# Kernel optimization log

Hardware: AMD Instinct MI355X
Metric: run time of the kernel (lower is better)

The kernel has to match this reference:

```python
import jax, jax.numpy as jnp
import numpy as np

N1, N2, C, H = 512, 512, 256, 512

def setup_inputs() -> dict:
    key = jax.random.key(0)
    ks = jax.random.split(key, 8)
    std = 0.01
    return {
        "X": jax.random.normal(ks[0], (N1, C), dtype=jnp.float32),
        "Y": jax.random.normal(ks[1], (N2, C), dtype=jnp.float32),
        "W_sr": jax.random.normal(ks[2], (C, C), dtype=jnp.float32) * std,   # project_sr.weight
        "W_tg": jax.random.normal(ks[3], (C, C), dtype=jnp.float32) * std,   # project_tg.weight
        "W1": jax.random.normal(ks[4], (H, 2 * C), dtype=jnp.float32) * std, # fc_M[0].weight [512,512]
        "b1": jnp.zeros((H,), dtype=jnp.float32),                            # fc_M[0].bias
        "w2": jax.random.normal(ks[5], (1, H), dtype=jnp.float32) * std,     # fc_M[2].weight [1,512]
        "b2": jnp.zeros((1,), dtype=jnp.float32),                            # fc_M[2].bias
    }

def reference(X, Y, W_sr, W_tg, W1, b1, w2, b2):
    # Projections (Linear without bias): x @ W.T
    Xp = X @ W_sr.T  # [N1, C]
    Yp = Y @ W_tg.T  # [N2, C]
    # fc_M first layer acts on concat([X_k, Y_k], -1); split W1 into the
    # halves that multiply Xp and Yp respectively (mathematically identical
    # to materializing the [N1,N2,2C] concat, but avoids it).
    W1x, W1y = W1[:, :C], W1[:, C:]
    hx = Xp @ W1x.T                     # [N1, H]
    hy = Yp @ W1y.T                     # [N2, H]
    Hid = jax.nn.relu(hx[:, None, :] + hy[None, :, :] + b1)  # [N1, N2, H]
    M = Hid @ w2[0] + b2[0]             # [N1, N2]  (squeeze of last dim 1)
    return M
```

## Files before the change

kernel.cpp:

```cpp
#include <hip/hip_runtime.h>


__global__ __launch_bounds__(256) void gemm_nt(
    const float* __restrict__ A0, const float* __restrict__ A1,
    const float* __restrict__ B0, const float* __restrict__ B1,
    float* __restrict__ C0, float* __restrict__ C1,
    const float* __restrict__ bias1, int N, int ldb)
{
    const int z = blockIdx.z;
    const float* A = z ? A1 : A0;
    const float* B = z ? B1 : B0;
    float* Cc      = z ? C1 : C0;
    const float* bias = z ? bias1 : nullptr;

    __shared__ float As[32 * 34];
    __shared__ float Bs[32 * 68];

    const int t  = threadIdx.x;
    const int m0 = blockIdx.x * 32;
    const int n0 = blockIdx.y * 64;
    const int ti = t / 16;
    const int tj = t % 16;

    float acc[2][4] = {};

    for (int kt = 0; kt < 256; kt += 32) {
        {
            const int m  = t / 8;
            const int k4 = (t % 8) * 4;
            float4 v = *(const float4*)&A[(m0 + m) * 256 + kt + k4];
            As[(k4 + 0) * 34 + m] = v.x;
            As[(k4 + 1) * 34 + m] = v.y;
            As[(k4 + 2) * 34 + m] = v.z;
            As[(k4 + 3) * 34 + m] = v.w;
        }
        #pragma unroll
        for (int r = 0; r < 2; r++) {
            const int id = t + r * 256;
            const int n  = id / 8;
            const int k4 = (id % 8) * 4;
            float4 v = *(const float4*)&B[(n0 + n) * ldb + kt + k4];
            Bs[(k4 + 0) * 68 + n] = v.x;
            Bs[(k4 + 1) * 68 + n] = v.y;
            Bs[(k4 + 2) * 68 + n] = v.z;
            Bs[(k4 + 3) * 68 + n] = v.w;
        }
        __syncthreads();

        #pragma unroll 8
        for (int k = 0; k < 32; k++) {
            float2 a = *(float2*)&As[k * 34 + 2 * ti];
            float4 b = *(float4*)&Bs[k * 68 + 4 * tj];
            acc[0][0] += a.x * b.x;  acc[0][1] += a.x * b.y;
            acc[0][2] += a.x * b.z;  acc[0][3] += a.x * b.w;
            acc[1][0] += a.y * b.x;  acc[1][1] += a.y * b.y;
            acc[1][2] += a.y * b.z;  acc[1][3] += a.y * b.w;
        }
        __syncthreads();
    }

    float4 bv = {0.f, 0.f, 0.f, 0.f};
    if (bias) bv = *(const float4*)&bias[n0 + 4 * tj];
    #pragma unroll
    for (int mi = 0; mi < 2; mi++) {
        const int m = m0 + 2 * ti + mi;
        float4 r;
        r.x = acc[mi][0] + bv.x;
        r.y = acc[mi][1] + bv.y;
        r.z = acc[mi][2] + bv.z;
        r.w = acc[mi][3] + bv.w;
        *(float4*)&Cc[m * N + n0 + 4 * tj] = r;
    }
}

__global__ __launch_bounds__(256) void affinity_core(
    const float* __restrict__ hx, const float* __restrict__ hy,
    const float* __restrict__ w2, float* __restrict__ partial)
{
    __shared__ float xs[64 * 68];
    __shared__ float ys[64 * 68];
    __shared__ float ws2[64];

    const int t  = threadIdx.x;
    const int i0 = blockIdx.x * 64;
    const int j0 = blockIdx.y * 64;
    const int h0 = blockIdx.z * 64;
    const int ti = t / 16;
    const int tj = t % 16;

    #pragma unroll
    for (int s = 0; s < 4; s++) {
        const int id = t + s * 256;
        const int r  = id / 16;
        const int c4 = (id % 16) * 4;
        *(float4*)&xs[r * 68 + c4] = *(const float4*)&hx[(i0 + r) * 512 + h0 + c4];
        *(float4*)&ys[r * 68 + c4] = *(const float4*)&hy[(j0 + r) * 512 + h0 + c4];
    }
    if (t < 16) *(float4*)&ws2[t * 4] = *(const float4*)&w2[h0 + t * 4];
    __syncthreads();

    float acc[4][4] = {};
    const float* xr = xs + ti * 68;
    const float* yr = ys + tj * 68;

    #pragma unroll 2
    for (int h4 = 0; h4 < 16; h4++) {
        const int ho = h4 * 4;
        float4 w = *(const float4*)&ws2[ho];
        float4 x[4], y[4];
        #pragma unroll
        for (int m = 0; m < 4; m++) x[m] = *(const float4*)&xr[m * (16 * 68) + ho];
        #pragma unroll
        for (int n = 0; n < 4; n++) y[n] = *(const float4*)&yr[n * (16 * 68) + ho];
        #pragma unroll
        for (int m = 0; m < 4; m++) {
            #pragma unroll
            for (int n = 0; n < 4; n++) {
                acc[m][n] += fmaxf(x[m].x + y[n].x, 0.f) * w.x
                           + fmaxf(x[m].y + y[n].y, 0.f) * w.y
                           + fmaxf(x[m].z + y[n].z, 0.f) * w.z
                           + fmaxf(x[m].w + y[n].w, 0.f) * w.w;
            }
        }
    }

    float* p = partial + blockIdx.z * (512 * 512);
    #pragma unroll
    for (int m = 0; m < 4; m++) {
        #pragma unroll
        for (int n = 0; n < 4; n++) {
            p[(i0 + ti + 16 * m) * 512 + (j0 + tj + 16 * n)] = acc[m][n];
        }
    }
}

__global__ __launch_bounds__(256) void reduce8(
    const float* __restrict__ partial, const float* __restrict__ b2,
    float* __restrict__ out)
{
    const int idx = (blockIdx.x * 256 + threadIdx.x) * 4;
    const float bb = b2[0];
    float4 r = {bb, bb, bb, bb};
    #pragma unroll
    for (int s = 0; s < 8; s++) {
        float4 p = *(const float4*)&partial[s * 262144 + idx];
        r.x += p.x; r.y += p.y; r.z += p.z; r.w += p.w;
    }
    *(float4*)&out[idx] = r;
}

extern "C" void kernel_launch(void* const* d_in, const int* in_sizes, int n_in,
                              void* d_out, int out_size, void* d_ws, size_t ws_size,
                              hipStream_t stream) {
    const float* X    = (const float*)d_in[0];
    const float* Y    = (const float*)d_in[1];
    const float* W_sr = (const float*)d_in[2];
    const float* W_tg = (const float*)d_in[3];
    const float* W1   = (const float*)d_in[4];
    const float* b1   = (const float*)d_in[5];
    const float* w2   = (const float*)d_in[6];
    const float* b2   = (const float*)d_in[7];

    float* ws      = (float*)d_ws;
    float* Xp      = ws;
    float* Yp      = ws + 131072;
    float* hx      = ws + 262144;
    float* hy      = ws + 524288;
    float* partial = ws + 786432;
    float* out     = (float*)d_out;

    gemm_nt<<<dim3(16, 4, 2), 256, 0, stream>>>(X, Y, W_sr, W_tg, Xp, Yp,
                                                nullptr, 256, 256);
    gemm_nt<<<dim3(16, 8, 2), 256, 0, stream>>>(Xp, Yp, W1, W1 + 256, hx, hy,
                                                b1, 512, 512);
    affinity_core<<<dim3(8, 8, 8), 256, 0, stream>>>(hx, hy, w2, partial);
    reduce8<<<256, 256, 0, stream>>>(partial, b2, out);
}
```

Before: 116.3 us.

## Fuse all four stages into one cooperative kernel with grid syncs

Replaces the four separate launches (two projection GEMMs, the affinity core and the partial reduction) with a single cooperative kernel of 256 blocks that runs each stage in turn, separated by grid-wide syncs. The affinity stage now gives each block 128 hidden units in two 64-wide chunks, so only four partial slabs are written and reduced instead of eight. The aim is to remove launch overhead and inter-kernel gaps and to cut partial-buffer traffic. In exchange, the affinity stage drops from 512 to 256 blocks with more serial work per block, and each grid sync adds a barrier cost.

Measured after the change: 212.4 us. 1.83x slower.

```diff
diff --git a/kernel.cpp b/kernel.cpp
--- a/kernel.cpp
+++ b/kernel.cpp
@@ -1,24 +1,19 @@
 #include <hip/hip_runtime.h>
-
-
-__global__ __launch_bounds__(256) void gemm_nt(
-    const float* __restrict__ A0, const float* __restrict__ A1,
-    const float* __restrict__ B0, const float* __restrict__ B1,
-    float* __restrict__ C0, float* __restrict__ C1,
-    const float* __restrict__ bias1, int N, int ldb)
+#include <hip/hip_cooperative_groups.h>
+
+namespace cg = cooperative_groups;
+
+
+#define LDS_FLOATS (2 * 64 * 68 + 64)
+
+__device__ __forceinline__ void gemm_tile_32x64(
+    const float* __restrict__ A, const float* __restrict__ B,
+    float* __restrict__ C, const float* __restrict__ bias,
+    int m0, int n0, int N, int ldb, float* lds, int t)
 {
-    const int z = blockIdx.z;
-    const float* A = z ? A1 : A0;
-    const float* B = z ? B1 : B0;
-    float* Cc      = z ? C1 : C0;
-    const float* bias = z ? bias1 : nullptr;
-
-    __shared__ float As[32 * 34];
-    __shared__ float Bs[32 * 68];
-
-    const int t  = threadIdx.x;
-    const int m0 = blockIdx.x * 32;
-    const int n0 = blockIdx.y * 64;
+    float* As = lds;
+    float* Bs = lds + 32 * 34;
+
     const int ti = t / 16;
     const int tj = t % 16;
 
@@ -69,84 +64,127 @@
         r.y = acc[mi][1] + bv.y;
         r.z = acc[mi][2] + bv.z;
         r.w = acc[mi][3] + bv.w;
-        *(float4*)&Cc[m * N + n0 + 4 * tj] = r;
+        *(float4*)&C[m * N + n0 + 4 * tj] = r;
     }
 }
 
-__global__ __launch_bounds__(256) void affinity_core(
-    const float* __restrict__ hx, const float* __restrict__ hy,
-    const float* __restrict__ w2, float* __restrict__ partial)
+__global__ __launch_bounds__(256) void fused_affinity(
+    const float* __restrict__ X, const float* __restrict__ Y,
+    const float* __restrict__ W_sr, const float* __restrict__ W_tg,
+    const float* __restrict__ W1, const float* __restrict__ b1,
+    const float* __restrict__ w2, const float* __restrict__ b2,
+    float* __restrict__ ws, float* __restrict__ out)
 {
-    __shared__ float xs[64 * 68];
-    __shared__ float ys[64 * 68];
-    __shared__ float ws2[64];
-
-    const int t  = threadIdx.x;
-    const int i0 = blockIdx.x * 64;
-    const int j0 = blockIdx.y * 64;
-    const int h0 = blockIdx.z * 64;
-    const int ti = t / 16;
-    const int tj = t % 16;
-
-    #pragma unroll
-    for (int s = 0; s < 4; s++) {
-        const int id = t + s * 256;
-        const int r  = id / 16;
-        const int c4 = (id % 16) * 4;
-        *(float4*)&xs[r * 68 + c4] = *(const float4*)&hx[(i0 + r) * 512 + h0 + c4];
-        *(float4*)&ys[r * 68 + c4] = *(const float4*)&hy[(j0 + r) * 512 + h0 + c4];
-    }
-    if (t < 16) *(float4*)&ws2[t * 4] = *(const float4*)&w2[h0 + t * 4];
-    __syncthreads();
-
-    float acc[4][4] = {};
-    const float* xr = xs + ti * 68;
-    const float* yr = ys + tj * 68;
-
-    #pragma unroll 2
-    for (int h4 = 0; h4 < 16; h4++) {
-        const int ho = h4 * 4;
-        float4 w = *(const float4*)&ws2[ho];
-        float4 x[4], y[4];
-        #pragma unroll
-        for (int m = 0; m < 4; m++) x[m] = *(const float4*)&xr[m * (16 * 68) + ho];
-        #pragma unroll
-        for (int n = 0; n < 4; n++) y[n] = *(const float4*)&yr[n * (16 * 68) + ho];
+    cg::grid_group grid = cg::this_grid();
+
+    __shared__ float lds[LDS_FLOATS];
+
+    float* Xp      = ws;
+    float* Yp      = ws + 131072;
+    float* hx      = ws + 262144;
+    float* hy      = ws + 524288;
+    float* partial = ws + 786432;
+
+    const int b = blockIdx.x;
+    const int t = threadIdx.x;
+
+    if (b < 128) {
+        const int prob = b >> 6;
+        const int tile = b & 63;
+        const int m0 = (tile >> 2) * 32;
+        const int n0 = (tile & 3) * 64;
+        gemm_tile_32x64(prob ? Y : X, prob ? W_tg : W_sr,
+                        prob ? Yp : Xp, nullptr,
+                        m0, n0, 256, 256, lds, t);
+    }
+    grid.sync();
+
+    {
+        const int prob = b >> 7;
+        const int tile = b & 127;
+        const int m0 = (tile >> 3) * 32;
+        const int n0 = (tile & 7) * 64;
+        gemm_tile_32x64(prob ? Yp : Xp, W1 + prob * 256,
+                        prob ? hy : hx, prob ? b1 : nullptr,
+                        m0, n0, 512, 512, lds, t);
+    }
+    grid.sync();
+
+    {
+        float* xs  = lds;
+        float* ys  = lds + 64 * 68;
+        float* ws2 = lds + 2 * 64 * 68;
+
+        const int slab = b >> 6;
+        const int tile = b & 63;
+        const int i0 = (tile >> 3) * 64;
+        const int j0 = (tile & 7) * 64;
+        const int h0 = slab * 128;
+        const int ti = t / 16;
+        const int tj = t % 16;
+
+        float acc[4][4] = {};
+
+        for (int hc = 0; hc < 128; hc += 64) {
+            const int hb = h0 + hc;
+            #pragma unroll
+            for (int s = 0; s < 4; s++) {
+                const int id = t + s * 256;
+                const int r  = id / 16;
+                const int c4 = (id % 16) * 4;
+                *(float4*)&xs[r * 68 + c4] = *(const float4*)&hx[(i0 + r) * 512 + hb + c4];
+                *(float4*)&ys[r * 68 + c4] = *(const float4*)&hy[(j0 + r) * 512 + hb + c4];
+            }
+            if (t < 16) *(float4*)&ws2[t * 4] = *(const float4*)&w2[hb + t * 4];
+            __syncthreads();
+
+            const float* xr = xs + ti * 68;
+            const float* yr = ys + tj * 68;
+            #pragma unroll 2
+            for (int h4 = 0; h4 < 16; h4++) {
+                const int ho = h4 * 4;
+                float4 w = *(const float4*)&ws2[ho];
+                float4 x[4], y[4];
+                #pragma unroll
+                for (int m = 0; m < 4; m++) x[m] = *(const float4*)&xr[m * (16 * 68) + ho];
+                #pragma unroll
+                for (int n = 0; n < 4; n++) y[n] = *(const float4*)&yr[n * (16 * 68) + ho];
+                #pragma unroll
+                for (int m = 0; m < 4; m++) {
+                    #pragma unroll
+                    for (int n = 0; n < 4; n++) {
+                        acc[m][n] += fmaxf(x[m].x + y[n].x, 0.f) * w.x
+                                   + fmaxf(x[m].y + y[n].y, 0.f) * w.y
+                                   + fmaxf(x[m].z + y[n].z, 0.f) * w.z
+                                   + fmaxf(x[m].w + y[n].w, 0.f) * w.w;
+                    }
+                }
+            }
+            __syncthreads();
+        }
+
+        float* p = partial + slab * (512 * 512);
         #pragma unroll
         for (int m = 0; m < 4; m++) {
             #pragma unroll
             for (int n = 0; n < 4; n++) {
-                acc[m][n] += fmaxf(x[m].x + y[n].x, 0.f) * w.x
-                           + fmaxf(x[m].y + y[n].y, 0.f) * w.y
-                           + fmaxf(x[m].z + y[n].z, 0.f) * w.z
-                           + fmaxf(x[m].w + y[n].w, 0.f) * w.w;
+                p[(i0 + ti + 16 * m) * 512 + (j0 + tj + 16 * n)] = acc[m][n];
             }
         }
     }
-
-    float* p = partial + blockIdx.z * (512 * 512);
-    #pragma unroll
-    for (int m = 0; m < 4; m++) {
+    grid.sync();
+
+    {
+        const int idx = (b * 256 + t) * 4;
+        const float bb = b2[0];
+        float4 r = {bb, bb, bb, bb};
         #pragma unroll
-        for (int n = 0; n < 4; n++) {
-            p[(i0 + ti + 16 * m) * 512 + (j0 + tj + 16 * n)] = acc[m][n];
-        }
-    }
-}
-
-__global__ __launch_bounds__(256) void reduce8(
-    const float* __restrict__ partial, const float* __restrict__ b2,
-    float* __restrict__ out)
-{
-    const int idx = (blockIdx.x * 256 + threadIdx.x) * 4;
-    const float bb = b2[0];
-    float4 r = {bb, bb, bb, bb};
-    #pragma unroll
-    for (int s = 0; s < 8; s++) {
-        float4 p = *(const float4*)&partial[s * 262144 + idx];
-        r.x += p.x; r.y += p.y; r.z += p.z; r.w += p.w;
-    }
-    *(float4*)&out[idx] = r;
+        for (int s = 0; s < 4; s++) {
+            float4 p = *(const float4*)&partial[s * 262144 + idx];
+            r.x += p.x; r.y += p.y; r.z += p.z; r.w += p.w;
+        }
+        *(float4*)&out[idx] = r;
+    }
 }
 
 extern "C" void kernel_launch(void* const* d_in, const int* in_sizes, int n_in,
@@ -160,19 +198,12 @@
     const float* b1   = (const float*)d_in[5];
     const float* w2   = (const float*)d_in[6];
     const float* b2   = (const float*)d_in[7];
-
-    float* ws      = (float*)d_ws;
-    float* Xp      = ws;
-    float* Yp      = ws + 131072;
-    float* hx      = ws + 262144;
-    float* hy      = ws + 524288;
-    float* partial = ws + 786432;
-    float* out     = (float*)d_out;
-
-    gemm_nt<<<dim3(16, 4, 2), 256, 0, stream>>>(X, Y, W_sr, W_tg, Xp, Yp,
-                                                nullptr, 256, 256);
-    gemm_nt<<<dim3(16, 8, 2), 256, 0, stream>>>(Xp, Yp, W1, W1 + 256, hx, hy,
-                                                b1, 512, 512);
-    affinity_core<<<dim3(8, 8, 8), 256, 0, stream>>>(hx, hy, w2, partial);
-    reduce8<<<256, 256, 0, stream>>>(partial, b2, out);
+    float* ws  = (float*)d_ws;
+    float* out = (float*)d_out;
+
+    void* args[] = {(void*)&X, (void*)&Y, (void*)&W_sr, (void*)&W_tg,
+                    (void*)&W1, (void*)&b1, (void*)&w2, (void*)&b2,
+                    (void*)&ws, (void*)&out};
+    hipLaunchCooperativeKernel((void*)fused_affinity, dim3(256), dim3(256),
+                               args, 0, stream);
 }
```
